# Kernel tuning notes

Measured on AMD Instinct MI355X. Metric: run time of the kernel, lower is better.

The kernel has to match this reference:

```python
import jax, jax.numpy as jnp
import numpy as np

B, T, F, H = 4096, 128, 64, 32
SCALE = 0.05  # small init so relu-LSTM doesn't blow up over 128 steps


def setup_inputs() -> dict:
    key = jax.random.key(0)
    ks = jax.random.split(key, 7)
    return {
        "x": jax.random.normal(ks[0], (B, T, F), jnp.float32),
        "We": jax.random.normal(ks[1], (F, 4 * H), jnp.float32) * SCALE,
        "Ue": jax.random.normal(ks[2], (H, 4 * H), jnp.float32) * SCALE,
        "be": jnp.zeros((4 * H,), jnp.float32),
        "Wd": jax.random.normal(ks[3], (H, 4 * H), jnp.float32) * SCALE,
        "Ud": jax.random.normal(ks[4], (H, 4 * H), jnp.float32) * SCALE,
        "bd": jnp.zeros((4 * H,), jnp.float32),
        "Wout": jax.random.normal(ks[5], (H, F), jnp.float32) * SCALE,
        "bout": jnp.zeros((F,), jnp.float32),
    }


def _lstm_relu(x, W, U, b):
    """Keras LSTM with activation='relu', recurrent_activation='sigmoid'.
    x: [B,T,D]. Returns (h_T [B,H], h_seq [B,T,H]). Gate order: i,f,c,o."""
    Bx = x.shape[0]
    Hh = U.shape[0]
    xz = jnp.einsum('btd,dg->btg', x, W) + b  # precompute input projections

    def step(carry, zt):
        h, c = carry
        z = zt + h @ U
        i, f, g, o = jnp.split(z, 4, axis=-1)
        i = jax.nn.sigmoid(i)
        f = jax.nn.sigmoid(f)
        g = jax.nn.relu(g)
        o = jax.nn.sigmoid(o)
        c = f * c + i * g
        h = o * jax.nn.relu(c)
        return (h, c), h

    h0 = jnp.zeros((Bx, Hh), x.dtype)
    (hT, _), hs = jax.lax.scan(step, (h0, h0), jnp.swapaxes(xz, 0, 1))
    return hT, jnp.swapaxes(hs, 0, 1)


def reference(x, We, Ue, be, Wd, Ud, bd, Wout, bout):
    # Encoder: LSTM(32, relu, return_sequences=False) -> RepeatVector(T)
    hT, _ = _lstm_relu(x, We, Ue, be)                      # [B,H]
    z = jnp.broadcast_to(hT[:, None, :], (x.shape[0], x.shape[1], hT.shape[-1]))
    # Decoder: LSTM(32, relu, return_sequences=True) -> TimeDistributed(Dense(F))
    _, hs = _lstm_relu(z, Wd, Ud, bd)                      # [B,T,H]
    return jnp.einsum('bth,hf->btf', hs, Wout) + bout      # [B,T,F]
```

## Files before the change

### kernel.cpp

```cpp
#include <hip/hip_runtime.h>
#include <hip/hip_bf16.h>

#define B_ 4096
#define T_ 128
#define F_ 64
#define H_ 32
#define G_ 128

using short8 = __attribute__((ext_vector_type(8))) short;
using f32x4  = __attribute__((ext_vector_type(4))) float;
using uint2v = __attribute__((ext_vector_type(2))) unsigned int;
using uint4v = __attribute__((ext_vector_type(4))) unsigned int;

#define MFMA16(Af, Bf, Cf) __builtin_amdgcn_mfma_f32_16x16x32_bf16((Af), (Bf), (Cf), 0, 0, 0)

__device__ __forceinline__ float sigmoid_f(float z) {
    return __builtin_amdgcn_rcpf(1.0f + __expf(-z));
}
__device__ __forceinline__ unsigned short bfb(float f) {
    return __builtin_bit_cast(unsigned short, __float2bfloat16(f));
}
__device__ __forceinline__ unsigned int pk(float a, float b) {
    return (unsigned int)bfb(a) | ((unsigned int)bfb(b) << 16);
}

extern "C" __global__ __launch_bounds__(256, 1)
void lstm_ae(const float* __restrict__ x,
             const float* __restrict__ We,
             const float* __restrict__ Ue,
             const float* __restrict__ be,
             const float* __restrict__ Wd,
             const float* __restrict__ Ud,
             const float* __restrict__ bd,
             const float* __restrict__ Wout,
             const float* __restrict__ bout,
             float* __restrict__ out)
{
    const int  lane = threadIdx.x & 63;
    const int  w    = threadIdx.x >> 6;
    const bool con  = (w < 2);
    const int  rw   = w & 1;
    const int  g    = lane >> 4;
    const int  c    = lane & 15;
    const int  b0   = blockIdx.x << 4;

    __shared__ __align__(16) unsigned int hx[2][16 * 18];
    __shared__ __align__(16) f32x4 zxbuf[2][8][64];

    short8 ueF[4];
    short8 weF[4][2];
    f32x4  beC[4];
    short8 hfrag = (short8)0;
    float  cs[4] = {0.f, 0.f, 0.f, 0.f};
    f32x4  zxC[4];
    f32x4  xa, xb, xc, xd;

    const float* xr = x + (size_t)(b0 + c) * (T_ * F_);
    const int xo = 8 * g;

#define CVTX(xf0, xf1)                                   \
    {                                                    \
        _Pragma("unroll")                                \
        for (int i = 0; i < 4; ++i) {                    \
            xf0[i]     = (short)bfb(xa[i]);              \
            xf0[4 + i] = (short)bfb(xb[i]);              \
            xf1[i]     = (short)bfb(xc[i]);              \
            xf1[4 + i] = (short)bfb(xd[i]);              \
        }                                                \
    }

#define GATES4(ACC, OWN)                                 \
    {                                                    \
        float hv[4];                                     \
        _Pragma("unroll")                                \
        for (int r = 0; r < 4; ++r) {                    \
            float iv = sigmoid_f(ACC[0][r]);             \
            float fv = sigmoid_f(ACC[1][r]);             \
            float gv = fmaxf(ACC[2][r], 0.f);            \
            float ov = sigmoid_f(ACC[3][r]);             \
            float cc = fmaf(fv, cs[r], iv * gv);         \
            cs[r] = cc;                                  \
            hv[r] = ov * fmaxf(cc, 0.f);                 \
        }                                                \
        OWN.x = pk(hv[0], hv[1]);                        \
        OWN.y = pk(hv[2], hv[3]);                        \
    }

    if (con) {
#pragma unroll
        for (int q = 0; q < 4; ++q) {
            const int n = 2 * q + rw;
#pragma unroll
            for (int i = 0; i < 8; ++i)
                ueF[q][i] = (short)bfb(Ue[(4 * g + (i & 3) + 16 * (i >> 2)) * G_ + 16 * n + c]);
        }
    } else {
#pragma unroll
        for (int q = 0; q < 4; ++q) {
            const int n = 2 * q + rw;
#pragma unroll
            for (int kc = 0; kc < 2; ++kc)
#pragma unroll
                for (int i = 0; i < 8; ++i)
                    weF[q][kc][i] = (short)bfb(We[(kc * 32 + 8 * g + i) * G_ + 16 * n + c]);
            beC[q] = *(const f32x4*)(be + 16 * n + 4 * g);
        }
        xa = *(const f32x4*)(xr + xo);
        xb = *(const f32x4*)(xr + xo + 4);
        xc = *(const f32x4*)(xr + 32 + xo);
        xd = *(const f32x4*)(xr + 36 + xo);
        short8 xf0, xf1;
        CVTX(xf0, xf1)
#pragma unroll
        for (int q = 0; q < 4; ++q) {
            f32x4 z = MFMA16(weF[q][0], xf0, beC[q]);
            z = MFMA16(weF[q][1], xf1, z);
            zxbuf[0][2 * q + rw][lane] = z;
        }
        const float* xn = xr + F_;
        xa = *(const f32x4*)(xn + xo);
        xb = *(const f32x4*)(xn + xo + 4);
        xc = *(const f32x4*)(xn + 32 + xo);
        xd = *(const f32x4*)(xn + 36 + xo);
    }
    __syncthreads();
    if (con) {
#pragma unroll
        for (int q = 0; q < 4; ++q) zxC[q] = zxbuf[0][2 * q + rw][lane];
    }

#pragma unroll 1
    for (int t = 0; t < T_; ++t) {
        uint2v own;
        if (con) {
            f32x4 acc[4];
#pragma unroll
            for (int q = 0; q < 4; ++q)
                acc[q] = MFMA16(ueF[q], hfrag, zxC[q]);
            GATES4(acc, own)
            *(uint2v*)&hx[t & 1][c * 18 + 8 * rw + 2 * g] = own;
        } else if (t + 1 < T_) {
            short8 xf0, xf1;
            CVTX(xf0, xf1)
            if (t + 2 < T_) {
                const float* xn = xr + (t + 2) * F_;
                xa = *(const f32x4*)(xn + xo);
                xb = *(const f32x4*)(xn + xo + 4);
                xc = *(const f32x4*)(xn + 32 + xo);
                xd = *(const f32x4*)(xn + 36 + xo);
            }
#pragma unroll
            for (int q = 0; q < 4; ++q) {
                f32x4 z = MFMA16(weF[q][0], xf0, beC[q]);
                z = MFMA16(weF[q][1], xf1, z);
                zxbuf[(t + 1) & 1][2 * q + rw][lane] = z;
            }
        }
        __syncthreads();
        if (con) {
            uint2v oth = *(const uint2v*)&hx[t & 1][c * 18 + 8 * (1 - rw) + 2 * g];
            uint4v hb;
            hb.x = rw ? oth.x : own.x;
            hb.y = rw ? oth.y : own.y;
            hb.z = rw ? own.x : oth.x;
            hb.w = rw ? own.y : oth.y;
            hfrag = __builtin_bit_cast(short8, hb);
            if (t + 1 < T_) {
#pragma unroll
                for (int q = 0; q < 4; ++q)
                    zxC[q] = zxbuf[(t + 1) & 1][2 * q + rw][lane];
            }
        }
    }

    short8 udF[4];
    f32x4  zd[4];
    short8 woF[2];
    f32x4  boC[2];
    float* ob[4];
    if (con) {
        short8 wdF[4];
#pragma unroll
        for (int q = 0; q < 4; ++q) {
            const int n = 2 * q + rw;
#pragma unroll
            for (int i = 0; i < 8; ++i) {
                const int pr = 4 * g + (i & 3) + 16 * (i >> 2);
                wdF[q][i] = (short)bfb(Wd[pr * G_ + 16 * n + c]);
                udF[q][i] = (short)bfb(Ud[pr * G_ + 16 * n + c]);
            }
        }
#pragma unroll
        for (int q = 0; q < 4; ++q) {
            f32x4 tb = *(const f32x4*)(bd + 16 * (2 * q + rw) + 4 * g);
            zd[q] = MFMA16(wdF[q], hfrag, tb);
        }
        hfrag = (short8)0;
#pragma unroll
        for (int r = 0; r < 4; ++r) cs[r] = 0.f;
    } else {
#pragma unroll
        for (int mi = 0; mi < 2; ++mi) {
            const int m = 2 * rw + mi;
#pragma unroll
            for (int i = 0; i < 8; ++i)
                woF[mi][i] = (short)bfb(Wout[(4 * g + (i & 3) + 16 * (i >> 2)) * F_ + 16 * m + c]);
            float v = bout[16 * m + c];
            boC[mi][0] = v; boC[mi][1] = v; boC[mi][2] = v; boC[mi][3] = v;
        }
#pragma unroll
        for (int r = 0; r < 4; ++r)
            ob[r] = out + (size_t)(b0 + 4 * g + r) * (T_ * F_) + c;
    }

#pragma unroll 1
    for (int t = 0; t < T_; ++t) {
        uint2v own;
        if (con) {
            f32x4 acc[4];
#pragma unroll
            for (int q = 0; q < 4; ++q)
                acc[q] = MFMA16(udF[q], hfrag, zd[q]);
            GATES4(acc, own)
            *(uint2v*)&hx[t & 1][c * 18 + 8 * rw + 2 * g] = own;
        }
        __syncthreads();
        if (con) {
            uint2v oth = *(const uint2v*)&hx[t & 1][c * 18 + 8 * (1 - rw) + 2 * g];
            uint4v hb;
            hb.x = rw ? oth.x : own.x;
            hb.y = rw ? oth.y : own.y;
            hb.z = rw ? own.x : oth.x;
            hb.w = rw ? own.y : oth.y;
            hfrag = __builtin_bit_cast(short8, hb);
        } else {
            uint2v ha = *(const uint2v*)&hx[t & 1][c * 18 + 2 * g];
            uint2v hz = *(const uint2v*)&hx[t & 1][c * 18 + 8 + 2 * g];
            uint4v u; u.x = ha.x; u.y = ha.y; u.z = hz.x; u.w = hz.y;
            short8 hA = __builtin_bit_cast(short8, u);
#pragma unroll
            for (int mi = 0; mi < 2; ++mi) {
                f32x4 oac = MFMA16(hA, woF[mi], boC[mi]);
                const int m = 2 * rw + mi;
#pragma unroll
                for (int r = 0; r < 4; ++r)
                    ob[r][t * F_ + 16 * m] = oac[r];
            }
        }
    }
}

extern "C" void kernel_launch(void* const* d_in, const int* in_sizes, int n_in,
                              void* d_out, int out_size, void* d_ws, size_t ws_size,
                              hipStream_t stream) {
    (void)in_sizes; (void)n_in; (void)d_ws; (void)ws_size; (void)out_size;
    const float* x    = (const float*)d_in[0];
    const float* We   = (const float*)d_in[1];
    const float* Ue   = (const float*)d_in[2];
    const float* be   = (const float*)d_in[3];
    const float* Wd   = (const float*)d_in[4];
    const float* Ud   = (const float*)d_in[5];
    const float* bd   = (const float*)d_in[6];
    const float* Wout = (const float*)d_in[7];
    const float* bout = (const float*)d_in[8];
    float* out = (float*)d_out;

    dim3 grid(B_ / 16), block(256);
    hipLaunchKernelGGL(lstm_ae, grid, block, 0, stream,
                       x, We, Ue, be, Wd, Ud, bd, Wout, bout, out);
}
```

Before: 365.5 us.

## Merge producer/consumer waves into two waves doing projection, recurrence and output

Block size drops from four waves to two. Each wave now computes its own input projection (We·x) directly into the accumulator and does the recurrent step, removing the zxbuf shared-memory handoff. In the decoder, the same waves also do the output projection, reusing the h fragment from the previous step and deferring the output write by one step. This removes a role split and its shared-memory traffic, but puts the projection and output MFMAs plus the global loads on the serial critical path of the recurrence.

```diff
diff --git a/kernel.cpp b/kernel.cpp
--- a/kernel.cpp
+++ b/kernel.cpp
@@ -24,7 +24,7 @@
     return (unsigned int)bfb(a) | ((unsigned int)bfb(b) << 16);
 }
 
-extern "C" __global__ __launch_bounds__(256, 1)
+extern "C" __global__ __launch_bounds__(128, 1)
 void lstm_ae(const float* __restrict__ x,
              const float* __restrict__ We,
              const float* __restrict__ Ue,
@@ -36,27 +36,36 @@
              const float* __restrict__ bout,
              float* __restrict__ out)
 {
-    const int  lane = threadIdx.x & 63;
-    const int  w    = threadIdx.x >> 6;
-    const bool con  = (w < 2);
-    const int  rw   = w & 1;
-    const int  g    = lane >> 4;
-    const int  c    = lane & 15;
-    const int  b0   = blockIdx.x << 4;
+    const int lane = threadIdx.x & 63;
+    const int rw   = threadIdx.x >> 6;
+    const int g    = lane >> 4;
+    const int c    = lane & 15;
+    const int b0   = blockIdx.x << 4;
 
     __shared__ __align__(16) unsigned int hx[2][16 * 18];
-    __shared__ __align__(16) f32x4 zxbuf[2][8][64];
-
+
+    short8 weF[4][2];
     short8 ueF[4];
-    short8 weF[4][2];
     f32x4  beC[4];
+#pragma unroll
+    for (int q = 0; q < 4; ++q) {
+        const int n = 2 * q + rw;
+#pragma unroll
+        for (int kc = 0; kc < 2; ++kc)
+#pragma unroll
+            for (int i = 0; i < 8; ++i)
+                weF[q][kc][i] = (short)bfb(We[(kc * 32 + 8 * g + i) * G_ + 16 * n + c]);
+#pragma unroll
+        for (int i = 0; i < 8; ++i)
+            ueF[q][i] = (short)bfb(Ue[(4 * g + (i & 3) + 16 * (i >> 2)) * G_ + 16 * n + c]);
+        beC[q] = *(const f32x4*)(be + 16 * n + 4 * g);
+    }
+
+    const float* xr = x + (size_t)(b0 + c) * (T_ * F_);
+    const int xo = 8 * g;
+
     short8 hfrag = (short8)0;
     float  cs[4] = {0.f, 0.f, 0.f, 0.f};
-    f32x4  zxC[4];
-    f32x4  xa, xb, xc, xd;
-
-    const float* xr = x + (size_t)(b0 + c) * (T_ * F_);
-    const int xo = 8 * g;
 
 #define CVTX(xf0, xf1)                                   \
     {                                                    \
@@ -86,61 +95,38 @@
         OWN.y = pk(hv[2], hv[3]);                        \
     }
 
-    if (con) {
-#pragma unroll
-        for (int q = 0; q < 4; ++q) {
-            const int n = 2 * q + rw;
-#pragma unroll
-            for (int i = 0; i < 8; ++i)
-                ueF[q][i] = (short)bfb(Ue[(4 * g + (i & 3) + 16 * (i >> 2)) * G_ + 16 * n + c]);
-        }
-    } else {
-#pragma unroll
-        for (int q = 0; q < 4; ++q) {
-            const int n = 2 * q + rw;
-#pragma unroll
-            for (int kc = 0; kc < 2; ++kc)
-#pragma unroll
-                for (int i = 0; i < 8; ++i)
-                    weF[q][kc][i] = (short)bfb(We[(kc * 32 + 8 * g + i) * G_ + 16 * n + c]);
-            beC[q] = *(const f32x4*)(be + 16 * n + 4 * g);
-        }
-        xa = *(const f32x4*)(xr + xo);
-        xb = *(const f32x4*)(xr + xo + 4);
-        xc = *(const f32x4*)(xr + 32 + xo);
-        xd = *(const f32x4*)(xr + 36 + xo);
-        short8 xf0, xf1;
-        CVTX(xf0, xf1)
-#pragma unroll
-        for (int q = 0; q < 4; ++q) {
-            f32x4 z = MFMA16(weF[q][0], xf0, beC[q]);
-            z = MFMA16(weF[q][1], xf1, z);
-            zxbuf[0][2 * q + rw][lane] = z;
-        }
+    f32x4 xa = *(const f32x4*)(xr + xo);
+    f32x4 xb = *(const f32x4*)(xr + xo + 4);
+    f32x4 xc = *(const f32x4*)(xr + 32 + xo);
+    f32x4 xd = *(const f32x4*)(xr + 36 + xo);
+    short8 xf0, xf1;
+    CVTX(xf0, xf1)
+    {
         const float* xn = xr + F_;
         xa = *(const f32x4*)(xn + xo);
         xb = *(const f32x4*)(xn + xo + 4);
         xc = *(const f32x4*)(xn + 32 + xo);
         xd = *(const f32x4*)(xn + 36 + xo);
     }
-    __syncthreads();
-    if (con) {
-#pragma unroll
-        for (int q = 0; q < 4; ++q) zxC[q] = zxbuf[0][2 * q + rw][lane];
+    f32x4 acc[4];
+#pragma unroll
+    for (int q = 0; q < 4; ++q) {
+        acc[q] = MFMA16(weF[q][0], xf0, beC[q]);
+        acc[q] = MFMA16(weF[q][1], xf1, acc[q]);
     }
 
 #pragma unroll 1
     for (int t = 0; t < T_; ++t) {
+#pragma unroll
+        for (int q = 0; q < 4; ++q)
+            acc[q] = MFMA16(ueF[q], hfrag, acc[q]);
         uint2v own;
-        if (con) {
-            f32x4 acc[4];
-#pragma unroll
-            for (int q = 0; q < 4; ++q)
-                acc[q] = MFMA16(ueF[q], hfrag, zxC[q]);
-            GATES4(acc, own)
-            *(uint2v*)&hx[t & 1][c * 18 + 8 * rw + 2 * g] = own;
-        } else if (t + 1 < T_) {
-            short8 xf0, xf1;
+        GATES4(acc, own)
+        *(uint2v*)&hx[t & 1][c * 18 + 8 * rw + 2 * g] = own;
+        __syncthreads();
+
+        uint2v oth = *(const uint2v*)&hx[t & 1][c * 18 + 8 * (1 - rw) + 2 * g];
+        if (t + 1 < T_) {
             CVTX(xf0, xf1)
             if (t + 2 < T_) {
                 const float* xn = xr + (t + 2) * F_;
@@ -151,34 +137,21 @@
             }
 #pragma unroll
             for (int q = 0; q < 4; ++q) {
-                f32x4 z = MFMA16(weF[q][0], xf0, beC[q]);
-                z = MFMA16(weF[q][1], xf1, z);
-                zxbuf[(t + 1) & 1][2 * q + rw][lane] = z;
-            }
-        }
-        __syncthreads();
-        if (con) {
-            uint2v oth = *(const uint2v*)&hx[t & 1][c * 18 + 8 * (1 - rw) + 2 * g];
-            uint4v hb;
-            hb.x = rw ? oth.x : own.x;
-            hb.y = rw ? oth.y : own.y;
-            hb.z = rw ? own.x : oth.x;
-            hb.w = rw ? own.y : oth.y;
-            hfrag = __builtin_bit_cast(short8, hb);
-            if (t + 1 < T_) {
-#pragma unroll
-                for (int q = 0; q < 4; ++q)
-                    zxC[q] = zxbuf[(t + 1) & 1][2 * q + rw][lane];
-            }
-        }
-    }
-
-    short8 udF[4];
-    f32x4  zd[4];
-    short8 woF[2];
-    f32x4  boC[2];
-    float* ob[4];
-    if (con) {
+                acc[q] = MFMA16(weF[q][0], xf0, beC[q]);
+                acc[q] = MFMA16(weF[q][1], xf1, acc[q]);
+            }
+        }
+        uint4v hb;
+        hb.x = rw ? oth.x : own.x;
+        hb.y = rw ? oth.y : own.y;
+        hb.z = rw ? own.x : oth.x;
+        hb.w = rw ? own.y : oth.y;
+        hfrag = __builtin_bit_cast(short8, hb);
+    }
+
+    short8 udF[4], woF[2];
+    f32x4  zd[4], boC[2];
+    {
         short8 wdF[4];
 #pragma unroll
         for (int q = 0; q < 4; ++q) {
@@ -195,10 +168,6 @@
             f32x4 tb = *(const f32x4*)(bd + 16 * (2 * q + rw) + 4 * g);
             zd[q] = MFMA16(wdF[q], hfrag, tb);
         }
-        hfrag = (short8)0;
-#pragma unroll
-        for (int r = 0; r < 4; ++r) cs[r] = 0.f;
-    } else {
 #pragma unroll
         for (int mi = 0; mi < 2; ++mi) {
             const int m = 2 * rw + mi;
@@ -208,45 +177,52 @@
             float v = bout[16 * m + c];
             boC[mi][0] = v; boC[mi][1] = v; boC[mi][2] = v; boC[mi][3] = v;
         }
-#pragma unroll
-        for (int r = 0; r < 4; ++r)
-            ob[r] = out + (size_t)(b0 + 4 * g + r) * (T_ * F_) + c;
-    }
+    }
+
+    hfrag = (short8)0;
+#pragma unroll
+    for (int r = 0; r < 4; ++r) cs[r] = 0.f;
+
+    float* ob[4];
+#pragma unroll
+    for (int r = 0; r < 4; ++r)
+        ob[r] = out + (size_t)(b0 + 4 * g + r) * (T_ * F_) + c;
 
 #pragma unroll 1
     for (int t = 0; t < T_; ++t) {
+#pragma unroll
+        for (int q = 0; q < 4; ++q)
+            acc[q] = MFMA16(udF[q], hfrag, zd[q]);
         uint2v own;
-        if (con) {
-            f32x4 acc[4];
-#pragma unroll
-            for (int q = 0; q < 4; ++q)
-                acc[q] = MFMA16(udF[q], hfrag, zd[q]);
-            GATES4(acc, own)
-            *(uint2v*)&hx[t & 1][c * 18 + 8 * rw + 2 * g] = own;
-        }
+        GATES4(acc, own)
+        *(uint2v*)&hx[t & 1][c * 18 + 8 * rw + 2 * g] = own;
         __syncthreads();
-        if (con) {
-            uint2v oth = *(const uint2v*)&hx[t & 1][c * 18 + 8 * (1 - rw) + 2 * g];
-            uint4v hb;
-            hb.x = rw ? oth.x : own.x;
-            hb.y = rw ? oth.y : own.y;
-            hb.z = rw ? own.x : oth.x;
-            hb.w = rw ? own.y : oth.y;
-            hfrag = __builtin_bit_cast(short8, hb);
-        } else {
-            uint2v ha = *(const uint2v*)&hx[t & 1][c * 18 + 2 * g];
-            uint2v hz = *(const uint2v*)&hx[t & 1][c * 18 + 8 + 2 * g];
-            uint4v u; u.x = ha.x; u.y = ha.y; u.z = hz.x; u.w = hz.y;
-            short8 hA = __builtin_bit_cast(short8, u);
+
+        uint2v oth = *(const uint2v*)&hx[t & 1][c * 18 + 8 * (1 - rw) + 2 * g];
+        if (t > 0) {
 #pragma unroll
             for (int mi = 0; mi < 2; ++mi) {
-                f32x4 oac = MFMA16(hA, woF[mi], boC[mi]);
+                f32x4 oac = MFMA16(hfrag, woF[mi], boC[mi]);
                 const int m = 2 * rw + mi;
 #pragma unroll
                 for (int r = 0; r < 4; ++r)
-                    ob[r][t * F_ + 16 * m] = oac[r];
-            }
-        }
+                    ob[r][(t - 1) * F_ + 16 * m] = oac[r];
+            }
+        }
+        uint4v hb;
+        hb.x = rw ? oth.x : own.x;
+        hb.y = rw ? oth.y : own.y;
+        hb.z = rw ? own.x : oth.x;
+        hb.w = rw ? own.y : oth.y;
+        hfrag = __builtin_bit_cast(short8, hb);
+    }
+#pragma unroll
+    for (int mi = 0; mi < 2; ++mi) {
+        f32x4 oac = MFMA16(hfrag, woF[mi], boC[mi]);
+        const int m = 2 * rw + mi;
+#pragma unroll
+        for (int r = 0; r < 4; ++r)
+            ob[r][(T_ - 1) * F_ + 16 * m] = oac[r];
     }
 }
 
@@ -265,7 +241,7 @@
     const float* bout = (const float*)d_in[8];
     float* out = (float*)d_out;
 
-    dim3 grid(B_ / 16), block(256);
+    dim3 grid(B_ / 16), block(128);
     hipLaunchKernelGGL(lstm_ae, grid, block, 0, stream,
                        x, We, Ue, be, Wd, Ud, bd, Wout, bout, out);
 }
```

Measured after the change: 392.8 us. 7.5% more time.
